# Performance work log

Measured on AMD Instinct MI355X. Metric: run time of the kernel, lower is better.

Reference implementation:

```python
import jax, jax.numpy as jnp
import numpy as np

B, D, N, MH, MV = 4, 1024, 2048, 1024, 1024

def setup_inputs() -> dict:
    key = jax.random.key(0)
    k1, k2, k3, k4, k5 = jax.random.split(key, 5)
    return {
        "x": jax.random.normal(k1, (B, D, N), dtype=jnp.float32),
        "W_Q": jax.random.normal(k2, (MH, D), dtype=jnp.float32),
        "W_K": jax.random.normal(k3, (MH, D), dtype=jnp.float32),
        "W_V": jax.random.normal(k4, (MV, D), dtype=jnp.float32),
        "W_O": jax.random.normal(k5, (D, MV), dtype=jnp.float32),
    }

def reference(x, W_Q, W_K, W_V, W_O):
    # x: [b, d, n] (feature-major). Projections: [b, m, n]
    q = jnp.einsum('hd,bdn->bhn', W_Q, x)
    k = jnp.einsum('hd,bdn->bhn', W_K, x)
    v = jnp.einsum('vd,bdn->bvn', W_V, x)
    # scores[b,i,j] = sum_h k[b,h,i] * q[b,h,j]  -> [b, n, n]; NOTE: no 1/sqrt scale (faithful)
    scores = jnp.einsum('bhi,bhj->bij', k, q)
    scores = jax.nn.softmax(scores, axis=-1)
    # v @ scores -> [b, m_V, n]
    attn = jnp.einsum('bvi,bij->bvj', v, scores)
    # W_O @ attn -> [b, d, n]
    return jnp.einsum('dv,bvj->bdj', W_O, attn)
```

## Files before the change

### kernel.cpp

```cpp
#include <hip/hip_runtime.h>
#include <cstddef>
#include <cstdint>

typedef unsigned short u16;
typedef __attribute__((ext_vector_type(8))) short bf16x8;
typedef __attribute__((ext_vector_type(8))) _Float16 f16x8;
typedef __attribute__((ext_vector_type(4))) float f32x4;

#define GLOBAL_AS __attribute__((address_space(1)))
#define LDS_AS __attribute__((address_space(3)))

__device__ __forceinline__ void async16(const u16* g, u16* l) {
    __builtin_amdgcn_global_load_lds((GLOBAL_AS const uint32_t*)g,
                                     (LDS_AS uint32_t*)l, 16, 0, 0);
}

__device__ __forceinline__ u16 f2bf(float f) {
    uint32_t u = __builtin_bit_cast(uint32_t, f);
    uint32_t r = (u + 0x7FFFu + ((u >> 16) & 1u)) >> 16;
    return (u16)r;
}

__global__ __launch_bounds__(256)
void wcast(const float4* __restrict__ src, u16* __restrict__ dst)
{
    int i = blockIdx.x * 256 + threadIdx.x;
    float4 v = src[i];
    ushort4 a = { f2bf(v.x), f2bf(v.y), f2bf(v.z), f2bf(v.w) };
    *(ushort4*)&dst[4 * (size_t)i] = a;
}

__global__ __launch_bounds__(256)
void tsplit_h2(const float* __restrict__ Sb, size_t sBatch,
               u16* __restrict__ Db, size_t dBatch, size_t plane,
               int R, int C)
{
    const float* S = Sb + blockIdx.z * sBatch;
    u16* D = Db + blockIdx.z * dBatch;
    __shared__ float t[32][33];
    int tx = threadIdx.x & 31, ty = threadIdx.x >> 5;
    int c0 = blockIdx.x * 32, r0 = blockIdx.y * 32;
    #pragma unroll
    for (int k = 0; k < 4; ++k)
        t[ty + 8 * k][tx] = S[(size_t)(r0 + ty + 8 * k) * C + c0 + tx];
    __syncthreads();
    #pragma unroll
    for (int k = 0; k < 4; ++k) {
        float a = t[tx][ty + 8 * k] * 64.0f;
        _Float16 h0 = (_Float16)a;
        _Float16 h1 = (_Float16)(a - (float)h0);
        size_t o = (size_t)(c0 + ty + 8 * k) * R + r0 + tx;
        D[o] = __builtin_bit_cast(u16, h0);
        D[plane + o] = __builtin_bit_cast(u16, h1);
    }
}

__global__ __launch_bounds__(256)
void tcast(const float* __restrict__ S, u16* __restrict__ D, int R, int C)
{
    __shared__ float t[32][33];
    int tx = threadIdx.x & 31, ty = threadIdx.x >> 5;
    int c0 = blockIdx.x * 32, r0 = blockIdx.y * 32;
    #pragma unroll
    for (int k = 0; k < 4; ++k)
        t[ty + 8 * k][tx] = S[(size_t)(r0 + ty + 8 * k) * C + c0 + tx];
    __syncthreads();
    #pragma unroll
    for (int k = 0; k < 4; ++k)
        D[(size_t)(c0 + ty + 8 * k) * R + r0 + tx] = f2bf(t[tx][ty + 8 * k]);
}

__global__ __launch_bounds__(256)
void tbf16(const u16* __restrict__ Sb, size_t sBatch, u16* __restrict__ Db, size_t dBatch)
{
    const u16* S = Sb + blockIdx.z * sBatch;
    u16* D = Db + blockIdx.z * dBatch;
    __shared__ u16 t[32][34];
    int tx = threadIdx.x & 31, ty = threadIdx.x >> 5;
    int c0 = blockIdx.x * 32, r0 = blockIdx.y * 32;
    #pragma unroll
    for (int k = 0; k < 4; ++k)
        t[ty + 8 * k][tx] = S[(size_t)(r0 + ty + 8 * k) * 2048 + c0 + tx];
    __syncthreads();
    #pragma unroll
    for (int k = 0; k < 4; ++k)
        D[(size_t)(c0 + ty + 8 * k) * 2048 + r0 + tx] = t[tx][ty + 8 * k];
}

#define MMF4(AF, BF)                                                                   \
    _Pragma("unroll") for (int i = 0; i < 4; ++i)                                      \
        _Pragma("unroll") for (int j = 0; j < 4; ++j)                                  \
            acc[i][j] = __builtin_amdgcn_mfma_f32_16x16x32_f16(AF[i], BF[j], acc[i][j], 0, 0, 0);
#define MMB4(AF, BF)                                                                   \
    _Pragma("unroll") for (int i = 0; i < 4; ++i)                                      \
        _Pragma("unroll") for (int j = 0; j < 4; ++j)                                  \
            acc[i][j] = __builtin_amdgcn_mfma_f32_16x16x32_bf16(AF[i], BF[j], acc[i][j], 0, 0, 0);

template<int TERMS, int EPI>
__global__ __launch_bounds__(256)
void gemm_big(const u16* __restrict__ Ab, size_t aBatch, size_t aPlane,
              const u16* __restrict__ Bb, size_t bBatch, size_t bPlane,
              void* __restrict__ Cb, size_t cBatch, size_t cPlane,
              int M, int N, int K)
{
    constexpr int RSZ = 4096;
    constexpr int BUF = (TERMS == 3 ? 4 : 2) * RSZ;
    __shared__ u16 lds[2 * BUF];
    const u16* A = Ab + blockIdx.z * aBatch;
    const u16* B = Bb + blockIdx.z * bBatch;
    const int tid = threadIdx.x;
    const int lane = tid & 63, wave = tid >> 6;
    const int m0 = blockIdx.y * 128, n0 = blockIdx.x * 128;
    const int l15 = lane & 15, q = lane >> 4;
    const int rm = (wave >> 1) * 64, rn = (wave & 1) * 64;

    int sr[2], sg[2], sbase[2];
    #pragma unroll
    for (int it = 0; it < 2; ++it) {
        int s = tid + it * 256;
        sr[it] = s >> 2;
        sg[it] = (s & 3) ^ ((sr[it] >> 1) & 3);
        sbase[it] = (it * 256 + wave * 64) * 8;
    }
    const int fsw = (q ^ ((l15 >> 1) & 3)) * 8;
    int aoff[4], boff[4];
    #pragma unroll
    for (int f = 0; f < 4; ++f) {
        aoff[f] = (rm + f * 16 + l15) * 32 + fsw;
        boff[f] = (rn + f * 16 + l15) * 32 + fsw;
    }

    f32x4 acc[4][4];
    #pragma unroll
    for (int i = 0; i < 4; ++i)
        #pragma unroll
        for (int j = 0; j < 4; ++j)
            acc[i][j] = (f32x4){0.f, 0.f, 0.f, 0.f};

#define STAGEB(PP, KT)                                                                 \
    do {                                                                               \
        _Pragma("unroll")                                                              \
        for (int it = 0; it < 2; ++it) {                                               \
            const size_t ao = (size_t)(m0 + sr[it]) * K + (KT) + sg[it] * 8;           \
            const size_t bo = (size_t)(n0 + sr[it]) * K + (KT) + sg[it] * 8;           \
            const int d = (PP) * BUF + sbase[it];                                      \
            if (TERMS == 3) {                                                          \
                async16(A + ao, &lds[d]);                                              \
                async16(A + aPlane + ao, &lds[d + RSZ]);                               \
                async16(B + bo, &lds[d + 2 * RSZ]);                                    \
                async16(B + bPlane + bo, &lds[d + 3 * RSZ]);                           \
            } else {                                                                   \
                async16(A + ao, &lds[d]);                                              \
                async16(B + bo, &lds[d + RSZ]);                                        \
            }                                                                          \
        }                                                                              \
    } while (0)

    STAGEB(0, 0);
    for (int kt = 0; kt < K; kt += 32) {
        const int p = (kt >> 5) & 1;
        __syncthreads();
        if (kt + 32 < K) STAGEB(p ^ 1, kt + 32);
        const u16* L = &lds[p * BUF];
        if (TERMS == 3) {
            f16x8 a0f[4], b0f[4], xf[4];
            #pragma unroll
            for (int f = 0; f < 4; ++f) a0f[f] = *(const f16x8*)&L[aoff[f]];
            #pragma unroll
            for (int f = 0; f < 4; ++f) b0f[f] = *(const f16x8*)&L[2 * RSZ + boff[f]];
            MMF4(a0f, b0f);
            #pragma unroll
            for (int f = 0; f < 4; ++f) xf[f] = *(const f16x8*)&L[3 * RSZ + boff[f]];
            MMF4(a0f, xf);
            #pragma unroll
            for (int f = 0; f < 4; ++f) xf[f] = *(const f16x8*)&L[RSZ + aoff[f]];
            MMF4(xf, b0f);
        } else {
            bf16x8 af[4], bf_[4];
            #pragma unroll
            for (int f = 0; f < 4; ++f) af[f] = *(const bf16x8*)&L[aoff[f]];
            #pragma unroll
            for (int f = 0; f < 4; ++f) bf_[f] = *(const bf16x8*)&L[RSZ + boff[f]];
            MMB4(af, bf_);
        }
    }
#undef STAGEB

    #pragma unroll
    for (int i = 0; i < 4; ++i) {
        int row = m0 + rm + i * 16 + q * 4;
        #pragma unroll
        for (int j = 0; j < 4; ++j) {
            int col = n0 + rn + j * 16 + l15;
            #pragma unroll
            for (int r = 0; r < 4; ++r) {
                float v = acc[i][j][r];
                size_t o = (size_t)(row + r) * N + col;
                if (EPI == 0) {
                    ((float*)Cb + blockIdx.z * cBatch)[o] = v;
                } else if (EPI == 1) {
                    u16* C0 = (u16*)Cb + blockIdx.z * cBatch;
                    float vs = v * 0.000244140625f;
                    _Float16 h0 = (_Float16)vs;
                    _Float16 h1 = (_Float16)(vs - (float)h0);
                    C0[o] = __builtin_bit_cast(u16, h0);
                    C0[cPlane + o] = __builtin_bit_cast(u16, h1);
                } else {
                    ((u16*)Cb + blockIdx.z * cBatch)[o] = f2bf(v);
                }
            }
        }
    }
}

template<int TERMS, int EPI, int TM, int TN, int WGM, int WGN>
__global__ __launch_bounds__(512, 2)
void gemm_w(const u16* __restrict__ Ab, size_t aBatch, size_t aPlane,
            const u16* __restrict__ Bb, size_t bBatch, size_t bPlane,
            void* __restrict__ Cb, size_t cBatch, size_t cPlane,
            int M, int N, int K)
{
    constexpr int ASZ = TM * 32;
    constexpr int BSZ = TN * 32;
    constexpr int APL = (TERMS == 3) ? 2 : 1;
    constexpr int BUF = APL * (ASZ + BSZ);
    constexpr int FM = TM / WGM / 16;
    constexpr int FN = TN / WGN / 16;
    constexpr int AIT = ASZ / (512 * 8);
    constexpr int BIT = BSZ / (512 * 8);
    extern __shared__ __align__(16) u16 lds[];

    const u16* A = Ab + blockIdx.z * aBatch;
    const u16* B = Bb + blockIdx.z * bBatch;
    const int tid = threadIdx.x;
    const int lane = tid & 63, wave = tid >> 6;
    const int m0 = blockIdx.y * TM, n0 = blockIdx.x * TN;
    const int l15 = lane & 15, q = lane >> 4;
    const int rm = (wave / WGN) * (TM / WGM);
    const int rn = (wave % WGN) * (TN / WGN);

    const int fsw = (q ^ ((l15 >> 1) & 3)) * 8;
    int aoff[FM], boff[FN];
    #pragma unroll
    for (int f = 0; f < FM; ++f) aoff[f] = (rm + f * 16 + l15) * 32 + fsw;
    #pragma unroll
    for (int f = 0; f < FN; ++f) boff[f] = (rn + f * 16 + l15) * 32 + fsw;

    f32x4 acc[FM][FN];
    #pragma unroll
    for (int i = 0; i < FM; ++i)
        #pragma unroll
        for (int j = 0; j < FN; ++j)
            acc[i][j] = (f32x4){0.f, 0.f, 0.f, 0.f};

    auto stage = [&](int pp, int kt) {
        #pragma unroll
        for (int it = 0; it < AIT; ++it) {
            int s = tid + it * 512;
            int r = s >> 2;
            int g = (s & 3) ^ ((r >> 1) & 3);
            int base = pp * BUF + (it * 512 + wave * 64) * 8;
            size_t go = (size_t)(m0 + r) * K + kt + g * 8;
            async16(A + go, &lds[base]);
            if (TERMS == 3) async16(A + aPlane + go, &lds[base + ASZ]);
        }
        #pragma unroll
        for (int it = 0; it < BIT; ++it) {
            int s = tid + it * 512;
            int r = s >> 2;
            int g = (s & 3) ^ ((r >> 1) & 3);
            int base = pp * BUF + APL * ASZ + (it * 512 + wave * 64) * 8;
            size_t go = (size_t)(n0 + r) * K + kt + g * 8;
            async16(B + go, &lds[base]);
            if (TERMS == 3) async16(B + bPlane + go, &lds[base + BSZ]);
        }
    };

    stage(0, 0);
    for (int kt = 0; kt < K; kt += 32) {
        const int p = (kt >> 5) & 1;
        __syncthreads();
        if (kt + 32 < K) stage(p ^ 1, kt + 32);
        const u16* L = &lds[p * BUF];
        if (TERMS == 3) {
            f16x8 a0f[FM], b0f[FN], ax[FM], bx[FN];
            #pragma unroll
            for (int f = 0; f < FM; ++f) a0f[f] = *(const f16x8*)&L[aoff[f]];
            #pragma unroll
            for (int f = 0; f < FN; ++f) b0f[f] = *(const f16x8*)&L[APL * ASZ + boff[f]];
            #pragma unroll
            for (int i = 0; i < FM; ++i)
                #pragma unroll
                for (int j = 0; j < FN; ++j)
                    acc[i][j] = __builtin_amdgcn_mfma_f32_16x16x32_f16(a0f[i], b0f[j], acc[i][j], 0, 0, 0);
            #pragma unroll
            for (int f = 0; f < FN; ++f) bx[f] = *(const f16x8*)&L[APL * ASZ + BSZ + boff[f]];
            #pragma unroll
            for (int i = 0; i < FM; ++i)
                #pragma unroll
                for (int j = 0; j < FN; ++j)
                    acc[i][j] = __builtin_amdgcn_mfma_f32_16x16x32_f16(a0f[i], bx[j], acc[i][j], 0, 0, 0);
            #pragma unroll
            for (int f = 0; f < FM; ++f) ax[f] = *(const f16x8*)&L[ASZ + aoff[f]];
            #pragma unroll
            for (int i = 0; i < FM; ++i)
                #pragma unroll
                for (int j = 0; j < FN; ++j)
                    acc[i][j] = __builtin_amdgcn_mfma_f32_16x16x32_f16(ax[i], b0f[j], acc[i][j], 0, 0, 0);
        } else {
            bf16x8 af[FM], bf_[FN];
            #pragma unroll
            for (int f = 0; f < FM; ++f) af[f] = *(const bf16x8*)&L[aoff[f]];
            #pragma unroll
            for (int f = 0; f < FN; ++f) bf_[f] = *(const bf16x8*)&L[ASZ + boff[f]];
            #pragma unroll
            for (int i = 0; i < FM; ++i)
                #pragma unroll
                for (int j = 0; j < FN; ++j)
                    acc[i][j] = __builtin_amdgcn_mfma_f32_16x16x32_bf16(af[i], bf_[j], acc[i][j], 0, 0, 0);
        }
    }

    #pragma unroll
    for (int i = 0; i < FM; ++i) {
        int row = m0 + rm + i * 16 + q * 4;
        #pragma unroll
        for (int j = 0; j < FN; ++j) {
            int col = n0 + rn + j * 16 + l15;
            #pragma unroll
            for (int r = 0; r < 4; ++r) {
                float v = acc[i][j][r];
                size_t o = (size_t)(row + r) * N + col;
                if (EPI == 0) {
                    ((float*)Cb + blockIdx.z * cBatch)[o] = v;
                } else if (EPI == 1) {
                    u16* C0 = (u16*)Cb + blockIdx.z * cBatch;
                    float vs = v * 0.000244140625f;
                    _Float16 h0 = (_Float16)vs;
                    _Float16 h1 = (_Float16)(vs - (float)h0);
                    C0[o] = __builtin_bit_cast(u16, h0);
                    C0[cPlane + o] = __builtin_bit_cast(u16, h1);
                } else {
                    ((u16*)Cb + blockIdx.z * cBatch)[o] = f2bf(v);
                }
            }
        }
    }
}

__global__ __launch_bounds__(256)
void softmax_p(const float* __restrict__ Sb, size_t sBatch, u16* __restrict__ Pb, size_t pBatch)
{
    const float* S = Sb + blockIdx.y * sBatch + (size_t)blockIdx.x * 2048;
    u16* P = Pb + blockIdx.y * pBatch + (size_t)blockIdx.x * 2048;
    const int tid = threadIdx.x;

    float4 v0 = *(const float4*)&S[tid * 4];
    float4 v1 = *(const float4*)&S[1024 + tid * 4];

    float m = fmaxf(fmaxf(fmaxf(v0.x, v0.y), fmaxf(v0.z, v0.w)),
                    fmaxf(fmaxf(v1.x, v1.y), fmaxf(v1.z, v1.w)));
    #pragma unroll
    for (int off = 32; off > 0; off >>= 1)
        m = fmaxf(m, __shfl_xor(m, off, 64));
    __shared__ float redm[4];
    if ((tid & 63) == 0) redm[tid >> 6] = m;
    __syncthreads();
    m = fmaxf(fmaxf(redm[0], redm[1]), fmaxf(redm[2], redm[3]));

    v0.x = __expf(v0.x - m); v0.y = __expf(v0.y - m);
    v0.z = __expf(v0.z - m); v0.w = __expf(v0.w - m);
    v1.x = __expf(v1.x - m); v1.y = __expf(v1.y - m);
    v1.z = __expf(v1.z - m); v1.w = __expf(v1.w - m);

    float s = v0.x + v0.y + v0.z + v0.w + v1.x + v1.y + v1.z + v1.w;
    #pragma unroll
    for (int off = 32; off > 0; off >>= 1)
        s += __shfl_xor(s, off, 64);
    __shared__ float reds[4];
    if ((tid & 63) == 0) reds[tid >> 6] = s;
    __syncthreads();
    s = reds[0] + reds[1] + reds[2] + reds[3];

    const float r = 1.0f / s;
    ushort4 o0 = { f2bf(v0.x * r), f2bf(v0.y * r), f2bf(v0.z * r), f2bf(v0.w * r) };
    ushort4 o1 = { f2bf(v1.x * r), f2bf(v1.y * r), f2bf(v1.z * r), f2bf(v1.w * r) };
    *(ushort4*)&P[tid * 4] = o0;
    *(ushort4*)&P[1024 + tid * 4] = o1;
}

extern "C" void kernel_launch(void* const* d_in, const int* in_sizes, int n_in,
                              void* d_out, int out_size, void* d_ws, size_t ws_size,
                              hipStream_t stream)
{
    const size_t MB = 1048576;
    const size_t WREG = 34 * MB;
    const size_t PER  = 32 * MB;
    const size_t PER_US = PER / 2, PER_F = PER / 4;

    char* ws = (char*)d_ws;
    u16* WQT2 = (u16*)ws;
    u16* WKT2 = (u16*)(ws + 4 * MB);
    u16* M2   = (u16*)(ws + 8 * MB);
    u16* WObf = (u16*)(ws + 12 * MB);
    u16* WVT  = (u16*)(ws + 14 * MB);
    u16* WOV  = (u16*)(ws + 16 * MB);
    u16* xbf  = (u16*)(ws + 18 * MB);

    int G = (ws_size >= WREG + 4 * PER) ? 4 : (ws_size >= WREG + 2 * PER) ? 2 : 1;

    const float* x = (const float*)d_in[0];
    float* out = (float*)d_out;
    dim3 blk(256);

    hipFuncSetAttribute((const void*)gemm_w<3, 0, 256, 256, 2, 4>,
                        hipFuncAttributeMaxDynamicSharedMemorySize, 131072);
    hipFuncSetAttribute((const void*)gemm_w<3, 1, 256, 128, 4, 2>,
                        hipFuncAttributeMaxDynamicSharedMemorySize, 98304);

    tsplit_h2<<<dim3(32, 32, 1), blk, 0, stream>>>((const float*)d_in[1], 0, WQT2, 0, 1048576, 1024, 1024);
    tsplit_h2<<<dim3(32, 32, 1), blk, 0, stream>>>((const float*)d_in[2], 0, WKT2, 0, 1048576, 1024, 1024);
    gemm_big<3, 1><<<dim3(8, 8, 1), blk, 0, stream>>>(WKT2, 0, 1048576, WQT2, 0, 1048576,
                                                      M2, 0, 1048576, 1024, 1024, 1024);
    wcast<<<1024, blk, 0, stream>>>((const float4*)d_in[4], WObf);
    tcast<<<dim3(32, 32, 1), blk, 0, stream>>>((const float*)d_in[3], WVT, 1024, 1024);
    gemm_big<1, 2><<<dim3(8, 8, 1), blk, 0, stream>>>(WObf, 0, 0, WVT, 0, 0,
                                                      WOV, 0, 0, 1024, 1024, 1024);
    wcast<<<8192, blk, 0, stream>>>((const float4*)x, xbf);

    for (int b0 = 0; b0 < 4; b0 += G) {
        char* R = ws + WREG;
        u16*   xT2 = (u16*)R;
        u16*   TT2 = (u16*)(R + 8 * MB);
        float* S32 = (float*)(R + 16 * MB);
        u16*   Pb  = (u16*)R;
        u16*   PTb = (u16*)(R + 8 * MB);
        u16*   XPT = (u16*)(R + 16 * MB);

        tsplit_h2<<<dim3(64, 32, G), blk, 0, stream>>>(x + (size_t)b0 * 2097152, 2097152,
                                                       xT2, PER_US, 2097152, 1024, 2048);
        gemm_w<3, 1, 256, 128, 4, 2><<<dim3(8, 8, G), 512, 98304, stream>>>(
            xT2, PER_US, 2097152, M2, 0, 1048576, TT2, PER_US, 2097152, 2048, 1024, 1024);
        gemm_w<3, 0, 256, 256, 2, 4><<<dim3(8, 8, G), 512, 131072, stream>>>(
            xT2, PER_US, 2097152, TT2, PER_US, 2097152, S32, PER_F, 0, 2048, 2048, 1024);
        softmax_p<<<dim3(2048, G), blk, 0, stream>>>(S32, PER_F, Pb, PER_US);
        tbf16<<<dim3(64, 64, G), blk, 0, stream>>>(Pb, PER_US, PTb, PER_US);
        gemm_w<1, 2, 256, 128, 4, 2><<<dim3(8, 8, G), 512, 49152, stream>>>(
            PTb, PER_US, 0, xbf + (size_t)b0 * 2097152, 2097152, 0,
            XPT, PER_US, 0, 2048, 1024, 2048);
        gemm_w<1, 0, 256, 128, 4, 2><<<dim3(16, 4, G), 512, 49152, stream>>>(
            WOV, 0, 0, XPT, PER_US, 0, out + (size_t)b0 * 2097152, 2097152, 0,
            1024, 2048, 1024);
    }
}
```

Before: 416.1 us.

## Switch gemm_w to 32x32x16 MFMA, swizzle block order, fuse x casts

The wide GEMM kernel now uses 32x32x16 MFMA instructions with 16-float accumulators per fragment instead of 16x16x32. Each 32-wide K tile is consumed in two halves using the existing XOR-swizzled LDS layout. The kernel also remaps block IDs into 4x2 groups for better L2 reuse. Separately, the bf16 cast of x is fused into the split-transpose kernel, so x is read once per batch group. The larger instruction tile aims to cut LDS fragment reads per MFMA, at the cost of more accumulator registers and a more complex output row mapping.

```diff
diff --git a/kernel.cpp b/kernel.cpp
--- a/kernel.cpp
+++ b/kernel.cpp
@@ -6,6 +6,7 @@
 typedef __attribute__((ext_vector_type(8))) short bf16x8;
 typedef __attribute__((ext_vector_type(8))) _Float16 f16x8;
 typedef __attribute__((ext_vector_type(4))) float f32x4;
+typedef __attribute__((ext_vector_type(16))) float f32x16;
 
 #define GLOBAL_AS __attribute__((address_space(1)))
 #define LDS_AS __attribute__((address_space(3)))
@@ -50,6 +51,35 @@
         _Float16 h0 = (_Float16)a;
         _Float16 h1 = (_Float16)(a - (float)h0);
         size_t o = (size_t)(c0 + ty + 8 * k) * R + r0 + tx;
+        D[o] = __builtin_bit_cast(u16, h0);
+        D[plane + o] = __builtin_bit_cast(u16, h1);
+    }
+}
+
+__global__ __launch_bounds__(256)
+void xprep(const float* __restrict__ Sb, size_t sBatch,
+           u16* __restrict__ BFb, size_t bfBatch,
+           u16* __restrict__ Db, size_t dBatch, size_t plane)
+{
+    const float* S = Sb + blockIdx.z * sBatch;
+    u16* BF = BFb + blockIdx.z * bfBatch;
+    u16* D = Db + blockIdx.z * dBatch;
+    __shared__ float t[32][33];
+    int tx = threadIdx.x & 31, ty = threadIdx.x >> 5;
+    int c0 = blockIdx.x * 32, r0 = blockIdx.y * 32;
+    #pragma unroll
+    for (int k = 0; k < 4; ++k) {
+        float v = S[(size_t)(r0 + ty + 8 * k) * 2048 + c0 + tx];
+        t[ty + 8 * k][tx] = v;
+        BF[(size_t)(r0 + ty + 8 * k) * 2048 + c0 + tx] = f2bf(v);
+    }
+    __syncthreads();
+    #pragma unroll
+    for (int k = 0; k < 4; ++k) {
+        float a = t[tx][ty + 8 * k] * 64.0f;
+        _Float16 h0 = (_Float16)a;
+        _Float16 h1 = (_Float16)(a - (float)h0);
+        size_t o = (size_t)(c0 + ty + 8 * k) * 1024 + r0 + tx;
         D[o] = __builtin_bit_cast(u16, h0);
         D[plane + o] = __builtin_bit_cast(u16, h1);
     }
@@ -224,34 +254,40 @@
     constexpr int BSZ = TN * 32;
     constexpr int APL = (TERMS == 3) ? 2 : 1;
     constexpr int BUF = APL * (ASZ + BSZ);
-    constexpr int FM = TM / WGM / 16;
-    constexpr int FN = TN / WGN / 16;
-    constexpr int AIT = ASZ / (512 * 8);
-    constexpr int BIT = BSZ / (512 * 8);
+    constexpr int FM = TM / WGM / 32;
+    constexpr int FN = TN / WGN / 32;
+    constexpr int AIT = TM / 128;
+    constexpr int BIT = TN / 128;
     extern __shared__ __align__(16) u16 lds[];
+
+    int bid = blockIdx.x + gridDim.x * blockIdx.y;
+    int cpr = gridDim.x >> 2;
+    int c8 = bid & 7, kk = bid >> 3;
+    int bx = (kk % cpr) * 4 + (c8 & 3);
+    int by = (kk / cpr) * 2 + (c8 >> 2);
 
     const u16* A = Ab + blockIdx.z * aBatch;
     const u16* B = Bb + blockIdx.z * bBatch;
     const int tid = threadIdx.x;
     const int lane = tid & 63, wave = tid >> 6;
-    const int m0 = blockIdx.y * TM, n0 = blockIdx.x * TN;
-    const int l15 = lane & 15, q = lane >> 4;
+    const int m0 = by * TM, n0 = bx * TN;
+    const int l31 = lane & 31, half = lane >> 5;
     const int rm = (wave / WGN) * (TM / WGM);
     const int rn = (wave % WGN) * (TN / WGN);
 
-    const int fsw = (q ^ ((l15 >> 1) & 3)) * 8;
-    int aoff[FM], boff[FN];
-    #pragma unroll
-    for (int f = 0; f < FM; ++f) aoff[f] = (rm + f * 16 + l15) * 32 + fsw;
-    #pragma unroll
-    for (int f = 0; f < FN; ++f) boff[f] = (rn + f * 16 + l15) * 32 + fsw;
-
-    f32x4 acc[FM][FN];
+    int arow[FM], asw[FM], brow[FN], bsw[FN];
+    #pragma unroll
+    for (int f = 0; f < FM; ++f) { arow[f] = rm + f * 32 + l31; asw[f] = (arow[f] >> 1) & 3; }
+    #pragma unroll
+    for (int f = 0; f < FN; ++f) { brow[f] = rn + f * 32 + l31; bsw[f] = (brow[f] >> 1) & 3; }
+
+    f32x16 acc[FM][FN];
     #pragma unroll
     for (int i = 0; i < FM; ++i)
         #pragma unroll
         for (int j = 0; j < FN; ++j)
-            acc[i][j] = (f32x4){0.f, 0.f, 0.f, 0.f};
+            #pragma unroll
+            for (int r = 0; r < 16; ++r) acc[i][j][r] = 0.f;
 
     auto stage = [&](int pp, int kt) {
         #pragma unroll
@@ -282,55 +318,64 @@
         __syncthreads();
         if (kt + 32 < K) stage(p ^ 1, kt + 32);
         const u16* L = &lds[p * BUF];
-        if (TERMS == 3) {
-            f16x8 a0f[FM], b0f[FN], ax[FM], bx[FN];
-            #pragma unroll
-            for (int f = 0; f < FM; ++f) a0f[f] = *(const f16x8*)&L[aoff[f]];
-            #pragma unroll
-            for (int f = 0; f < FN; ++f) b0f[f] = *(const f16x8*)&L[APL * ASZ + boff[f]];
-            #pragma unroll
-            for (int i = 0; i < FM; ++i)
-                #pragma unroll
-                for (int j = 0; j < FN; ++j)
-                    acc[i][j] = __builtin_amdgcn_mfma_f32_16x16x32_f16(a0f[i], b0f[j], acc[i][j], 0, 0, 0);
-            #pragma unroll
-            for (int f = 0; f < FN; ++f) bx[f] = *(const f16x8*)&L[APL * ASZ + BSZ + boff[f]];
-            #pragma unroll
-            for (int i = 0; i < FM; ++i)
-                #pragma unroll
-                for (int j = 0; j < FN; ++j)
-                    acc[i][j] = __builtin_amdgcn_mfma_f32_16x16x32_f16(a0f[i], bx[j], acc[i][j], 0, 0, 0);
-            #pragma unroll
-            for (int f = 0; f < FM; ++f) ax[f] = *(const f16x8*)&L[ASZ + aoff[f]];
-            #pragma unroll
-            for (int i = 0; i < FM; ++i)
-                #pragma unroll
-                for (int j = 0; j < FN; ++j)
-                    acc[i][j] = __builtin_amdgcn_mfma_f32_16x16x32_f16(ax[i], b0f[j], acc[i][j], 0, 0, 0);
-        } else {
-            bf16x8 af[FM], bf_[FN];
-            #pragma unroll
-            for (int f = 0; f < FM; ++f) af[f] = *(const bf16x8*)&L[aoff[f]];
-            #pragma unroll
-            for (int f = 0; f < FN; ++f) bf_[f] = *(const bf16x8*)&L[ASZ + boff[f]];
-            #pragma unroll
-            for (int i = 0; i < FM; ++i)
-                #pragma unroll
-                for (int j = 0; j < FN; ++j)
-                    acc[i][j] = __builtin_amdgcn_mfma_f32_16x16x32_bf16(af[i], bf_[j], acc[i][j], 0, 0, 0);
+        #pragma unroll
+        for (int h = 0; h < 2; ++h) {
+            if (TERMS == 3) {
+                f16x8 a0[FM], b0[FN], tx[FM > FN ? FM : FN];
+                #pragma unroll
+                for (int f = 0; f < FM; ++f)
+                    a0[f] = *(const f16x8*)&L[arow[f] * 32 + ((2 * h + half) ^ asw[f]) * 8];
+                #pragma unroll
+                for (int f = 0; f < FN; ++f)
+                    b0[f] = *(const f16x8*)&L[APL * ASZ + brow[f] * 32 + ((2 * h + half) ^ bsw[f]) * 8];
+                #pragma unroll
+                for (int i = 0; i < FM; ++i)
+                    #pragma unroll
+                    for (int j = 0; j < FN; ++j)
+                        acc[i][j] = __builtin_amdgcn_mfma_f32_32x32x16_f16(a0[i], b0[j], acc[i][j], 0, 0, 0);
+                #pragma unroll
+                for (int f = 0; f < FN; ++f)
+                    tx[f] = *(const f16x8*)&L[APL * ASZ + BSZ + brow[f] * 32 + ((2 * h + half) ^ bsw[f]) * 8];
+                #pragma unroll
+                for (int i = 0; i < FM; ++i)
+                    #pragma unroll
+                    for (int j = 0; j < FN; ++j)
+                        acc[i][j] = __builtin_amdgcn_mfma_f32_32x32x16_f16(a0[i], tx[j], acc[i][j], 0, 0, 0);
+                #pragma unroll
+                for (int f = 0; f < FM; ++f)
+                    tx[f] = *(const f16x8*)&L[ASZ + arow[f] * 32 + ((2 * h + half) ^ asw[f]) * 8];
+                #pragma unroll
+                for (int i = 0; i < FM; ++i)
+                    #pragma unroll
+                    for (int j = 0; j < FN; ++j)
+                        acc[i][j] = __builtin_amdgcn_mfma_f32_32x32x16_f16(tx[i], b0[j], acc[i][j], 0, 0, 0);
+            } else {
+                bf16x8 a0[FM], b0[FN];
+                #pragma unroll
+                for (int f = 0; f < FM; ++f)
+                    a0[f] = *(const bf16x8*)&L[arow[f] * 32 + ((2 * h + half) ^ asw[f]) * 8];
+                #pragma unroll
+                for (int f = 0; f < FN; ++f)
+                    b0[f] = *(const bf16x8*)&L[ASZ + brow[f] * 32 + ((2 * h + half) ^ bsw[f]) * 8];
+                #pragma unroll
+                for (int i = 0; i < FM; ++i)
+                    #pragma unroll
+                    for (int j = 0; j < FN; ++j)
+                        acc[i][j] = __builtin_amdgcn_mfma_f32_32x32x16_bf16(a0[i], b0[j], acc[i][j], 0, 0, 0);
+            }
         }
     }
 
     #pragma unroll
     for (int i = 0; i < FM; ++i) {
-        int row = m0 + rm + i * 16 + q * 4;
         #pragma unroll
         for (int j = 0; j < FN; ++j) {
-            int col = n0 + rn + j * 16 + l15;
-            #pragma unroll
-            for (int r = 0; r < 4; ++r) {
+            int col = n0 + rn + j * 32 + l31;
+            #pragma unroll
+            for (int r = 0; r < 16; ++r) {
+                int row = m0 + rm + i * 32 + (r & 3) + 8 * (r >> 2) + 4 * half;
                 float v = acc[i][j][r];
-                size_t o = (size_t)(row + r) * N + col;
+                size_t o = (size_t)row * N + col;
                 if (EPI == 0) {
                     ((float*)Cb + blockIdx.z * cBatch)[o] = v;
                 } else if (EPI == 1) {
@@ -426,7 +471,6 @@
     tcast<<<dim3(32, 32, 1), blk, 0, stream>>>((const float*)d_in[3], WVT, 1024, 1024);
     gemm_big<1, 2><<<dim3(8, 8, 1), blk, 0, stream>>>(WObf, 0, 0, WVT, 0, 0,
                                                       WOV, 0, 0, 1024, 1024, 1024);
-    wcast<<<8192, blk, 0, stream>>>((const float4*)x, xbf);
 
     for (int b0 = 0; b0 < 4; b0 += G) {
         char* R = ws + WREG;
@@ -437,8 +481,9 @@
         u16*   PTb = (u16*)(R + 8 * MB);
         u16*   XPT = (u16*)(R + 16 * MB);
 
-        tsplit_h2<<<dim3(64, 32, G), blk, 0, stream>>>(x + (size_t)b0 * 2097152, 2097152,
-                                                       xT2, PER_US, 2097152, 1024, 2048);
+        xprep<<<dim3(64, 32, G), blk, 0, stream>>>(x + (size_t)b0 * 2097152, 2097152,
+                                                   xbf + (size_t)b0 * 2097152, 2097152,
+                                                   xT2, PER_US, 2097152);
         gemm_w<3, 1, 256, 128, 4, 2><<<dim3(8, 8, G), 512, 98304, stream>>>(
             xT2, PER_US, 2097152, M2, 0, 1048576, TT2, PER_US, 2097152, 2048, 1024, 1024);
         gemm_w<3, 0, 256, 256, 2, 4><<<dim3(8, 8, G), 512, 131072, stream>>>(
```

Measured after the change: 407.9 us. 2.0% less time.
